# Optimization experiments

Hardware: AMD Instinct MI355X
Metric: run time of the kernel (lower is better)

## Reference

```python
import jax, jax.numpy as jnp
import numpy as np

C = 256
INTER = C // 2


def _conv1x1(x, w, b):
    # x: [B,C,H,W], w: [O,C], b: [O] -> [B,O,H,W]
    return jnp.einsum('bchw,oc->bohw', x, w) + b[None, :, None, None]


def setup_inputs() -> dict:
    key = jax.random.key(0)
    ks = jax.random.split(key, 9)
    B, H, W = 4, 64, 64
    x = jax.random.normal(ks[0], (B, C, H, W), dtype=jnp.float32)
    s_in = 1.0 / np.sqrt(C)
    s_int = 1.0 / np.sqrt(INTER)
    return {
        'x': x,
        'w_g': jax.random.normal(ks[1], (INTER, C), jnp.float32) * s_in,
        'b_g': jax.random.normal(ks[2], (INTER,), jnp.float32) * 0.01,
        'w_theta': jax.random.normal(ks[3], (INTER, C), jnp.float32) * s_in,
        'b_theta': jax.random.normal(ks[4], (INTER,), jnp.float32) * 0.01,
        'w_phi': jax.random.normal(ks[5], (INTER, C), jnp.float32) * s_in,
        'b_phi': jax.random.normal(ks[6], (INTER,), jnp.float32) * 0.01,
        'w_W': jax.random.normal(ks[7], (C, INTER), jnp.float32) * s_int,
        'b_W': jax.random.normal(ks[8], (C,), jnp.float32) * 0.01,
    }


def reference(x, w_g, b_g, w_theta, b_theta, w_phi, b_phi, w_W, b_W):
    B, Cc, H, W = x.shape
    N = H * W
    # 1x1 conv projections -> flatten spatial to N
    g_x = _conv1x1(x, w_g, b_g).reshape(B, INTER, N).transpose(0, 2, 1)        # [B,N,I]
    theta_x = _conv1x1(x, w_theta, b_theta).reshape(B, INTER, N).transpose(0, 2, 1)  # [B,N,I]
    phi_x = _conv1x1(x, w_phi, b_phi).reshape(B, INTER, N)                     # [B,I,N]
    f = jnp.einsum('bni,bim->bnm', theta_x, phi_x)                             # [B,N,N]
    f_div_C = jax.nn.softmax(f, axis=-1)
    y = jnp.einsum('bnm,bmi->bni', f_div_C, g_x)                               # [B,N,I]
    y = y.transpose(0, 2, 1).reshape(B, INTER, H, W)
    W_y = _conv1x1(y, w_W, b_W)                                                # [B,C,H,W]
    return W_y + x
```

## Files before the change

### kernel.cpp

```cpp
#include <hip/hip_runtime.h>

typedef unsigned short ushort_t;
typedef unsigned int uint_t;
typedef _Float16 f16;
typedef __attribute__((ext_vector_type(8))) _Float16 f16x8;
typedef __attribute__((ext_vector_type(2))) _Float16 f16x2;
typedef __attribute__((ext_vector_type(4))) float f32x4;

#define B_ 4
#define C_ 256
#define I_ 128
#define N_ 4096
#define SPLITS 4
#define KV_PER (N_ / SPLITS)
#define KVB 64
#define NIT (KV_PER / KVB)

#define XT_HI 0ull
#define XT_LO 4194304ull
#define W_F   8388608ull
#define TH_F  8519680ull
#define PH_F  10616832ull
#define G2_F  12713984ull
#define YP_OFF 0ull
#define YM_OFF TH_F
#define LSE_BYTE_OFF 29622272ull

__device__ __forceinline__ f16x2 pkrtz(float a, float b) {
    auto r = __builtin_amdgcn_cvt_pkrtz(a, b);
    f16x2 o;
    __builtin_memcpy(&o, &r, sizeof(o));
    return o;
}
__device__ __forceinline__ f32x4 mfma16h(f16x8 a, f16x8 b, f32x4 c) {
    return __builtin_amdgcn_mfma_f32_16x16x32_f16(a, b, c, 0, 0, 0);
}
__device__ __forceinline__ f32x4 zero4() { f32x4 z = {0.f, 0.f, 0.f, 0.f}; return z; }
__device__ __forceinline__ void gload_lds16(const void* g, void* lds) {
    __builtin_amdgcn_global_load_lds(
        (const __attribute__((address_space(1))) void*)g,
        (__attribute__((address_space(3))) void*)lds, 16, 0, 0);
}

__global__ __launch_bounds__(256) void k_convert_w(const float* wg, const float* wt,
                                                   const float* wp, const float* wW,
                                                   ushort_t* ws) {
    int idx = blockIdx.x * 256 + threadIdx.x;
    float v;
    if (idx < 32768)        v = wg[idx];
    else if (idx < 65536)   v = wt[idx - 32768];
    else if (idx < 98304)   v = wp[idx - 65536];
    else                    v = wW[idx - 98304];
    ((f16*)(ws + W_F))[idx] = (f16)v;
}

__global__ __launch_bounds__(256) void k_transpose_x(const float* x, ushort_t* ws) {
    __shared__ float t[64][65];
    int b = blockIdx.z, c0 = blockIdx.y * 64, n0 = blockIdx.x * 64;
    int tid = threadIdx.x;
    int cl = tid & 63, ng = tid >> 6;
    const float* xp = x + ((size_t)(b * C_ + c0 + cl)) * N_ + n0 + ng * 16;
#pragma unroll
    for (int j = 0; j < 4; ++j) {
        float4 v = ((const float4*)xp)[j];
        t[cl][ng * 16 + j * 4 + 0] = v.x;
        t[cl][ng * 16 + j * 4 + 1] = v.y;
        t[cl][ng * 16 + j * 4 + 2] = v.z;
        t[cl][ng * 16 + j * 4 + 3] = v.w;
    }
    __syncthreads();
    int nl = tid & 63, cg = tid >> 6;
    f16 hv[16], lv[16];
#pragma unroll
    for (int k = 0; k < 16; ++k) {
        float v = t[cg * 16 + k][nl];
        f16 h = (f16)v;
        hv[k] = h;
        lv[k] = (f16)(v - (float)h);
    }
    size_t dst = ((size_t)b * N_ + n0 + nl) * C_ + c0 + cg * 16;
    *(uint4*)&ws[XT_HI + dst]     = *(uint4*)&hv[0];
    *(uint4*)&ws[XT_HI + dst + 8] = *(uint4*)&hv[8];
    *(uint4*)&ws[XT_LO + dst]     = *(uint4*)&lv[0];
    *(uint4*)&ws[XT_LO + dst + 8] = *(uint4*)&lv[8];
}

__global__ __launch_bounds__(512) void k_proj_all(const float* bg, const float* bth,
                                                  const float* bph, ushort_t* ws) {
    int b = blockIdx.y, n0 = blockIdx.x * 64;
    int w = threadIdx.x >> 6, l = threadIdx.x & 63;
    int li = l & 15, lg = l >> 4;
    int wn = (w & 3) * 16;
    int ihb = (w >> 2) * 4;
    const f16* xh = (const f16*)(ws + XT_HI);
    const f16* xl = (const f16*)(ws + XT_LO);
    const f16* wf = (const f16*)(ws + W_F);

    f32x4 acc[3][4];
#pragma unroll
    for (int p = 0; p < 3; ++p)
#pragma unroll
        for (int t = 0; t < 4; ++t) acc[p][t] = zero4();

    size_t arow = ((size_t)b * N_ + n0 + wn + li) * C_;
#pragma unroll 2
    for (int kb = 0; kb < 8; ++kb) {
        int kc = kb * 32 + 8 * lg;
        f16x8 ah = *(const f16x8*)&xh[arow + kc];
        f16x8 al = *(const f16x8*)&xl[arow + kc];
#pragma unroll
        for (int p = 0; p < 3; ++p)
#pragma unroll
            for (int t = 0; t < 4; ++t) {
                f16x8 bw = *(const f16x8*)&wf[(size_t)p * 32768 + (size_t)((ihb + t) * 16 + li) * C_ + kc];
                acc[p][t] = mfma16h(ah, bw, acc[p][t]);
                acc[p][t] = mfma16h(al, bw, acc[p][t]);
            }
    }
    f16* g2p = (f16*)(ws + G2_F);
    f16* thp = (f16*)(ws + TH_F);
    f16* php = (f16*)(ws + PH_F);
#pragma unroll
    for (int p = 0; p < 3; ++p) {
        const float* bias = (p == 0) ? bg : (p == 1) ? bth : bph;
#pragma unroll
        for (int t = 0; t < 4; ++t) {
            int i = (ihb + t) * 16 + li;
            float bs = bias[i];
#pragma unroll
            for (int r = 0; r < 4; ++r) {
                int n = n0 + wn + 4 * lg + r;
                float v = acc[p][t][r] + bs;
                if (p == 0)
                    g2p[(((size_t)b * (N_ / 4) + (n >> 2)) * I_ + i) * 4 + (n & 3)] = (f16)v;
                else if (p == 1)
                    thp[((size_t)b * N_ + n) * I_ + i] = (f16)v;
                else
                    php[((size_t)b * N_ + n) * I_ + i] = (f16)v;
            }
        }
    }
}

__global__ __launch_bounds__(512, 4) void k_attn(ushort_t* ws, float* lse) {
    __shared__ __align__(16) ushort_t smem[32768];
    int b = blockIdx.y, sp = blockIdx.z;
    int w = threadIdx.x >> 6, l = threadIdx.x & 63;
    int li = l & 15, lg = l >> 4;
    int q0 = blockIdx.x * 128 + w * 16;
    const f16* th = (const f16*)(ws + TH_F);
    const f16* ph = (const f16*)(ws + PH_F);
    const f16* g2 = (const f16*)(ws + G2_F);
    f16* yp = (f16*)(ws + YP_OFF) + (size_t)sp * ((size_t)B_ * N_ * I_);

    f16x8 qf[4];
#pragma unroll
    for (int kb = 0; kb < 4; ++kb)
        qf[kb] = *(const f16x8*)&th[((size_t)b * N_ + q0 + li) * I_ + kb * 32 + 8 * lg];

    f32x4 y[8];
#pragma unroll
    for (int dt = 0; dt < 8; ++dt) y[dt] = zero4();
    float m = -1e30f, ls = 0.f;

    int kv_beg = sp * KV_PER;
    int srow = l >> 4;
    size_t sp0 = ((size_t)b * N_ + w * 8 + srow) * I_ + ((l & 15) ^ srow) * 8;
    size_t sp1 = ((size_t)b * N_ + w * 8 + 4 + srow) * I_ + (((l & 15) ^ srow) ^ 4) * 8;
    size_t sg0 = ((size_t)b * (N_ / 4) + w * 2) * (I_ * 4) + l * 8;
    int dp = w * 1024;
    int dg = 16384 + w * 1024;

    auto stage = [&](int kv0, int bufsel) {
        int bo = bufsel ? 8192 : 0;
        gload_lds16(ph + sp0 + (size_t)kv0 * I_, smem + bo + dp);
        gload_lds16(ph + sp1 + (size_t)kv0 * I_, smem + bo + dp + 512);
        gload_lds16(g2 + sg0 + (size_t)kv0 * 128, smem + bo + dg);
        gload_lds16(g2 + sg0 + (size_t)kv0 * 128 + 512, smem + bo + dg + 512);
    };

    stage(kv_beg, 0);
    __syncthreads();

    for (int it = 0; it < NIT; ++it) {
        int buf = it & 1;
        if (it + 1 < NIT) stage(kv_beg + (it + 1) * KVB, buf ^ 1);
        const f16* pbuf = (const f16*)(smem + (buf ? 8192 : 0));
        const f16* gbuf = (const f16*)(smem + 16384 + (buf ? 8192 : 0));

        f32x4 f[4];
#pragma unroll
        for (int h = 0; h < 4; ++h) f[h] = zero4();
        __builtin_amdgcn_s_setprio(1);
#pragma unroll
        for (int kb = 0; kb < 4; ++kb) {
            int cc = ((kb * 4 + lg) ^ (li & 7)) * 8;
#pragma unroll
            for (int h = 0; h < 4; ++h) {
                f16x8 a = *(const f16x8*)&pbuf[(h * 16 + li) * 128 + cc];
                f[h] = mfma16h(a, qf[kb], f[h]);
            }
        }
        __builtin_amdgcn_s_setprio(0);

        float tm = fmaxf(fmaxf(fmaxf(f[0][0], f[0][1]), fmaxf(f[0][2], f[0][3])),
                         fmaxf(fmaxf(f[1][0], f[1][1]), fmaxf(f[1][2], f[1][3])));
        tm = fmaxf(tm, fmaxf(fmaxf(fmaxf(f[2][0], f[2][1]), fmaxf(f[2][2], f[2][3])),
                             fmaxf(fmaxf(f[3][0], f[3][1]), fmaxf(f[3][2], f[3][3]))));
        tm = fmaxf(tm, __shfl_xor(tm, 16));
        tm = fmaxf(tm, __shfl_xor(tm, 32));
        if (__ballot(tm > m + 8.f)) {
            float mn = fmaxf(m, tm);
            float sc = __expf(m - mn);
            ls *= sc; m = mn;
            float s0 = __shfl(sc, 4 * lg + 0);
            float s1 = __shfl(sc, 4 * lg + 1);
            float s2 = __shfl(sc, 4 * lg + 2);
            float s3 = __shfl(sc, 4 * lg + 3);
#pragma unroll
            for (int dt = 0; dt < 8; ++dt) {
                y[dt][0] *= s0; y[dt][1] *= s1; y[dt][2] *= s2; y[dt][3] *= s3;
            }
        }
        float rs = 0.f;
#pragma unroll
        for (int h = 0; h < 4; ++h)
#pragma unroll
            for (int r = 0; r < 4; ++r) {
                f[h][r] = __expf(f[h][r] - m);
                rs += f[h][r];
            }
        rs += __shfl_xor(rs, 16);
        rs += __shfl_xor(rs, 32);
        ls += rs;

        union PU { f16x2 h2[4]; f16x8 v; };
        PU pA, pB;
        pA.h2[0] = pkrtz(f[0][0], f[0][1]); pA.h2[1] = pkrtz(f[0][2], f[0][3]);
        pA.h2[2] = pkrtz(f[1][0], f[1][1]); pA.h2[3] = pkrtz(f[1][2], f[1][3]);
        pB.h2[0] = pkrtz(f[2][0], f[2][1]); pB.h2[1] = pkrtz(f[2][2], f[2][3]);
        pB.h2[2] = pkrtz(f[3][0], f[3][1]); pB.h2[3] = pkrtz(f[3][2], f[3][3]);

        __builtin_amdgcn_s_setprio(1);
#pragma unroll
        for (int dt = 0; dt < 8; ++dt) {
            int i4 = (dt * 16 + li) * 4;
            union GU { uint_t u[4]; f16x8 v; };
            GU g0, g1;
            *(uint2*)&g0.u[0] = *(const uint2*)&gbuf[lg * 512 + i4];
            *(uint2*)&g0.u[2] = *(const uint2*)&gbuf[(4 + lg) * 512 + i4];
            y[dt] = mfma16h(pA.v, g0.v, y[dt]);
            *(uint2*)&g1.u[0] = *(const uint2*)&gbuf[(8 + lg) * 512 + i4];
            *(uint2*)&g1.u[2] = *(const uint2*)&gbuf[(12 + lg) * 512 + i4];
            y[dt] = mfma16h(pB.v, g1.v, y[dt]);
        }
        __builtin_amdgcn_s_setprio(0);
        __syncthreads();
    }

    float inv = 1.0f / ls;
    float i0 = __shfl(inv, 4 * lg + 0);
    float i1 = __shfl(inv, 4 * lg + 1);
    float i2 = __shfl(inv, 4 * lg + 2);
    float i3 = __shfl(inv, 4 * lg + 3);
#pragma unroll
    for (int dt = 0; dt < 8; ++dt) {
        size_t base = ((size_t)b * N_ + q0 + 4 * lg) * I_ + dt * 16 + li;
        yp[base]          = (f16)(y[dt][0] * i0);
        yp[base + I_]     = (f16)(y[dt][1] * i1);
        yp[base + 2 * I_] = (f16)(y[dt][2] * i2);
        yp[base + 3 * I_] = (f16)(y[dt][3] * i3);
    }
    if (l < 16)
        lse[((size_t)sp * B_ + b) * N_ + q0 + l] = m + __logf(ls);
}

__global__ __launch_bounds__(256) void k_merge(ushort_t* ws, const float* lse) {
    int t = blockIdx.x * 256 + threadIdx.x;
    size_t base = (size_t)t * 8;
    size_t row = base >> 7;
    float l0 = lse[row];
    float l1 = lse[(size_t)B_ * N_ + row];
    float l2 = lse[2 * (size_t)B_ * N_ + row];
    float l3 = lse[3 * (size_t)B_ * N_ + row];
    float mx = fmaxf(fmaxf(l0, l1), fmaxf(l2, l3));
    float w0 = __expf(l0 - mx), w1 = __expf(l1 - mx);
    float w2 = __expf(l2 - mx), w3 = __expf(l3 - mx);
    float inv = 1.0f / (w0 + w1 + w2 + w3);
    float wgt[4] = {w0 * inv, w1 * inv, w2 * inv, w3 * inv};
    const f16* yp = (const f16*)(ws + YP_OFF);
    const size_t STRIDE = (size_t)B_ * N_ * I_;
    float acc[8];
#pragma unroll
    for (int j = 0; j < 8; ++j) acc[j] = 0.f;
#pragma unroll
    for (int sp = 0; sp < 4; ++sp) {
        f16x8 v = *(const f16x8*)&yp[sp * STRIDE + base];
#pragma unroll
        for (int j = 0; j < 8; ++j) acc[j] += wgt[sp] * (float)v[j];
    }
    f16 o[8];
#pragma unroll
    for (int j = 0; j < 8; ++j) o[j] = (f16)acc[j];
    *(uint4*)&((f16*)(ws + YM_OFF))[base] = *(uint4*)&o[0];
}

__global__ __launch_bounds__(256) void k_out(const float* x, const float* bW,
                                             const ushort_t* ws, float* out) {
    int b = blockIdx.y, n0 = blockIdx.x * 64;
    int w = threadIdx.x >> 6, l = threadIdx.x & 63;
    int li = l & 15, lg = l >> 4;
    int cw = blockIdx.z * 128 + (w >> 1) * 64;
    int nh = (w & 1) * 32;
    const f16* wfp = (const f16*)(ws + W_F) + 98304;
    const f16* yb  = (const f16*)(ws + YM_OFF);

    f32x4 acc[4][2];
#pragma unroll
    for (int mm = 0; mm < 4; ++mm)
#pragma unroll
        for (int n = 0; n < 2; ++n) acc[mm][n] = zero4();

#pragma unroll 2
    for (int kb = 0; kb < 4; ++kb) {
        int kc = kb * 32 + 8 * lg;
        f16x8 a[4], byv[2];
#pragma unroll
        for (int mm = 0; mm < 4; ++mm)
            a[mm] = *(const f16x8*)&wfp[(size_t)(cw + mm * 16 + li) * I_ + kc];
#pragma unroll
        for (int n = 0; n < 2; ++n)
            byv[n] = *(const f16x8*)&yb[((size_t)b * N_ + n0 + nh + n * 16 + li) * I_ + kc];
#pragma unroll
        for (int mm = 0; mm < 4; ++mm)
#pragma unroll
            for (int n = 0; n < 2; ++n)
                acc[mm][n] = mfma16h(a[mm], byv[n], acc[mm][n]);
    }
#pragma unroll
    for (int mm = 0; mm < 4; ++mm)
#pragma unroll
        for (int n = 0; n < 2; ++n)
#pragma unroll
            for (int r = 0; r < 4; ++r) {
                int c = cw + mm * 16 + lg * 4 + r;
                int nn = n0 + nh + n * 16 + li;
                size_t xi = ((size_t)b * C_ + c) * N_ + nn;
                out[xi] = acc[mm][n][r] + bW[c] + x[xi];
            }
}

extern "C" void kernel_launch(void* const* d_in, const int* in_sizes, int n_in,
                              void* d_out, int out_size, void* d_ws, size_t ws_size,
                              hipStream_t stream) {
    const float* x  = (const float*)d_in[0];
    const float* wg = (const float*)d_in[1];
    const float* bg = (const float*)d_in[2];
    const float* wt = (const float*)d_in[3];
    const float* bt = (const float*)d_in[4];
    const float* wp = (const float*)d_in[5];
    const float* bp = (const float*)d_in[6];
    const float* wW = (const float*)d_in[7];
    const float* bW = (const float*)d_in[8];
    ushort_t* ws = (ushort_t*)d_ws;
    float* lse = (float*)((char*)d_ws + LSE_BYTE_OFF);
    float* out = (float*)d_out;

    k_convert_w<<<512, 256, 0, stream>>>(wg, wt, wp, wW, ws);
    k_transpose_x<<<dim3(64, 4, 4), 256, 0, stream>>>(x, ws);
    k_proj_all<<<dim3(64, 4), 512, 0, stream>>>(bg, bt, bp, ws);
    k_attn<<<dim3(32, 4, SPLITS), 512, 0, stream>>>(ws, lse);
    k_merge<<<1024, 256, 0, stream>>>(ws, lse);
    k_out<<<dim3(64, 4, 2), 256, 0, stream>>>(x, bW, ws, out);
}
```

Baseline: 119.6 us.

## Drop hi/lo x split, fuse weight convert and merge, retile attention with exp2

```diff
diff --git a/kernel.cpp b/kernel.cpp
--- a/kernel.cpp
+++ b/kernel.cpp
@@ -11,20 +11,18 @@
 #define C_ 256
 #define I_ 128
 #define N_ 4096
-#define SPLITS 4
-#define KV_PER (N_ / SPLITS)
-#define KVB 64
-#define NIT (KV_PER / KVB)
-
-#define XT_HI 0ull
-#define XT_LO 4194304ull
-#define W_F   8388608ull
-#define TH_F  8519680ull
-#define PH_F  10616832ull
-#define G2_F  12713984ull
-#define YP_OFF 0ull
-#define YM_OFF TH_F
-#define LSE_BYTE_OFF 29622272ull
+#define KVB 32
+#define LOG2E 1.44269504f
+
+#define XT_F 0ull
+#define W_F  4194304ull
+#define TH_F 4325376ull
+#define PH_F 6422528ull
+#define G2_F 8519680ull
+#define YP_F 10616832ull
+
+__device__ __forceinline__ float exp2_hw(float x) { return __builtin_amdgcn_exp2f(x); }
+__device__ __forceinline__ float log2_hw(float x) { return __builtin_amdgcn_logf(x); }
 
 __device__ __forceinline__ f16x2 pkrtz(float a, float b) {
     auto r = __builtin_amdgcn_cvt_pkrtz(a, b);
@@ -42,19 +40,25 @@
         (__attribute__((address_space(3))) void*)lds, 16, 0, 0);
 }
 
-__global__ __launch_bounds__(256) void k_convert_w(const float* wg, const float* wt,
-                                                   const float* wp, const float* wW,
-                                                   ushort_t* ws) {
-    int idx = blockIdx.x * 256 + threadIdx.x;
-    float v;
-    if (idx < 32768)        v = wg[idx];
-    else if (idx < 65536)   v = wt[idx - 32768];
-    else if (idx < 98304)   v = wp[idx - 65536];
-    else                    v = wW[idx - 98304];
-    ((f16*)(ws + W_F))[idx] = (f16)v;
-}
-
-__global__ __launch_bounds__(256) void k_transpose_x(const float* x, ushort_t* ws) {
+__global__ __launch_bounds__(256) void k_transpose_x(const float* x, const float* wg,
+        const float* wt, const float* wp, const float* wW, ushort_t* ws) {
+    if (blockIdx.x >= 64) {
+        int idx = (((blockIdx.x - 64) * 16 + blockIdx.y * 4 + blockIdx.z) * 256
+                   + threadIdx.x) * 16;
+        const float* src;
+        int off;
+        if (idx < 32768)      { src = wg; off = idx; }
+        else if (idx < 65536) { src = wt; off = idx - 32768; }
+        else if (idx < 98304) { src = wp; off = idx - 65536; }
+        else                  { src = wW; off = idx - 98304; }
+        f16 o[16];
+#pragma unroll
+        for (int j = 0; j < 16; ++j) o[j] = (f16)src[off + j];
+        f16* wd = (f16*)(ws + W_F);
+        *(uint4*)&wd[idx]     = *(uint4*)&o[0];
+        *(uint4*)&wd[idx + 8] = *(uint4*)&o[8];
+        return;
+    }
     __shared__ float t[64][65];
     int b = blockIdx.z, c0 = blockIdx.y * 64, n0 = blockIdx.x * 64;
     int tid = threadIdx.x;
@@ -70,19 +74,13 @@
     }
     __syncthreads();
     int nl = tid & 63, cg = tid >> 6;
-    f16 hv[16], lv[16];
-#pragma unroll
-    for (int k = 0; k < 16; ++k) {
-        float v = t[cg * 16 + k][nl];
-        f16 h = (f16)v;
-        hv[k] = h;
-        lv[k] = (f16)(v - (float)h);
-    }
+    f16 hv[16];
+#pragma unroll
+    for (int k = 0; k < 16; ++k) hv[k] = (f16)t[cg * 16 + k][nl];
     size_t dst = ((size_t)b * N_ + n0 + nl) * C_ + c0 + cg * 16;
-    *(uint4*)&ws[XT_HI + dst]     = *(uint4*)&hv[0];
-    *(uint4*)&ws[XT_HI + dst + 8] = *(uint4*)&hv[8];
-    *(uint4*)&ws[XT_LO + dst]     = *(uint4*)&lv[0];
-    *(uint4*)&ws[XT_LO + dst + 8] = *(uint4*)&lv[8];
+    f16* xd = (f16*)(ws + XT_F);
+    *(uint4*)&xd[dst]     = *(uint4*)&hv[0];
+    *(uint4*)&xd[dst + 8] = *(uint4*)&hv[8];
 }
 
 __global__ __launch_bounds__(512) void k_proj_all(const float* bg, const float* bth,
@@ -92,8 +90,7 @@
     int li = l & 15, lg = l >> 4;
     int wn = (w & 3) * 16;
     int ihb = (w >> 2) * 4;
-    const f16* xh = (const f16*)(ws + XT_HI);
-    const f16* xl = (const f16*)(ws + XT_LO);
+    const f16* xh = (const f16*)(ws + XT_F);
     const f16* wf = (const f16*)(ws + W_F);
 
     f32x4 acc[3][4];
@@ -107,14 +104,13 @@
     for (int kb = 0; kb < 8; ++kb) {
         int kc = kb * 32 + 8 * lg;
         f16x8 ah = *(const f16x8*)&xh[arow + kc];
-        f16x8 al = *(const f16x8*)&xl[arow + kc];
 #pragma unroll
         for (int p = 0; p < 3; ++p)
 #pragma unroll
             for (int t = 0; t < 4; ++t) {
-                f16x8 bw = *(const f16x8*)&wf[(size_t)p * 32768 + (size_t)((ihb + t) * 16 + li) * C_ + kc];
+                f16x8 bw = *(const f16x8*)&wf[(size_t)p * 32768
+                               + (size_t)((ihb + t) * 16 + li) * C_ + kc];
                 acc[p][t] = mfma16h(ah, bw, acc[p][t]);
-                acc[p][t] = mfma16h(al, bw, acc[p][t]);
             }
     }
     f16* g2p = (f16*)(ws + G2_F);
@@ -134,7 +130,7 @@
                 if (p == 0)
                     g2p[(((size_t)b * (N_ / 4) + (n >> 2)) * I_ + i) * 4 + (n & 3)] = (f16)v;
                 else if (p == 1)
-                    thp[((size_t)b * N_ + n) * I_ + i] = (f16)v;
+                    thp[((size_t)b * N_ + n) * I_ + i] = (f16)(v * LOG2E);
                 else
                     php[((size_t)b * N_ + n) * I_ + i] = (f16)v;
             }
@@ -142,8 +138,8 @@
     }
 }
 
-__global__ __launch_bounds__(512, 4) void k_attn(ushort_t* ws, float* lse) {
-    __shared__ __align__(16) ushort_t smem[32768];
+__global__ __launch_bounds__(256, 3) void k_attn(ushort_t* ws, float* lse, int splits) {
+    __shared__ __align__(16) ushort_t smem[16384];
     int b = blockIdx.y, sp = blockIdx.z;
     int w = threadIdx.x >> 6, l = threadIdx.x & 63;
     int li = l & 15, lg = l >> 4;
@@ -151,175 +147,219 @@
     const f16* th = (const f16*)(ws + TH_F);
     const f16* ph = (const f16*)(ws + PH_F);
     const f16* g2 = (const f16*)(ws + G2_F);
-    f16* yp = (f16*)(ws + YP_OFF) + (size_t)sp * ((size_t)B_ * N_ * I_);
-
-    f16x8 qf[4];
-#pragma unroll
-    for (int kb = 0; kb < 4; ++kb)
-        qf[kb] = *(const f16x8*)&th[((size_t)b * N_ + q0 + li) * I_ + kb * 32 + 8 * lg];
-
-    f32x4 y[8];
-#pragma unroll
-    for (int dt = 0; dt < 8; ++dt) y[dt] = zero4();
-    float m = -1e30f, ls = 0.f;
-
-    int kv_beg = sp * KV_PER;
+    f16* yp = (f16*)(ws + YP_F) + (size_t)sp * ((size_t)B_ * N_ * I_);
+
+    f16x8 qA[4], qB[4];
+#pragma unroll
+    for (int kb = 0; kb < 4; ++kb) {
+        qA[kb] = *(const f16x8*)&th[((size_t)b * N_ + q0 + li) * I_ + kb * 32 + 8 * lg];
+        qB[kb] = *(const f16x8*)&th[((size_t)b * N_ + q0 + 64 + li) * I_ + kb * 32 + 8 * lg];
+    }
+
+    f32x4 yA[8], yB[8];
+#pragma unroll
+    for (int dt = 0; dt < 8; ++dt) { yA[dt] = zero4(); yB[dt] = zero4(); }
+    float mA = -1e30f, lA = 0.f, mB = -1e30f, lB = 0.f;
+
+    int kvper = N_ / splits;
+    int kv_beg = sp * kvper, nit = kvper / KVB;
     int srow = l >> 4;
     size_t sp0 = ((size_t)b * N_ + w * 8 + srow) * I_ + ((l & 15) ^ srow) * 8;
     size_t sp1 = ((size_t)b * N_ + w * 8 + 4 + srow) * I_ + (((l & 15) ^ srow) ^ 4) * 8;
-    size_t sg0 = ((size_t)b * (N_ / 4) + w * 2) * (I_ * 4) + l * 8;
-    int dp = w * 1024;
-    int dg = 16384 + w * 1024;
+    size_t sg0 = ((size_t)b * (N_ / 4) + w * 2) * 512 + l * 8;
 
     auto stage = [&](int kv0, int bufsel) {
-        int bo = bufsel ? 8192 : 0;
-        gload_lds16(ph + sp0 + (size_t)kv0 * I_, smem + bo + dp);
-        gload_lds16(ph + sp1 + (size_t)kv0 * I_, smem + bo + dp + 512);
-        gload_lds16(g2 + sg0 + (size_t)kv0 * 128, smem + bo + dg);
-        gload_lds16(g2 + sg0 + (size_t)kv0 * 128 + 512, smem + bo + dg + 512);
+        int bo = bufsel * 4096;
+        gload_lds16(ph + (size_t)kv0 * I_ + sp0, smem + bo + w * 1024);
+        gload_lds16(ph + (size_t)kv0 * I_ + sp1, smem + bo + w * 1024 + 512);
+        gload_lds16(g2 + (size_t)(kv0 >> 2) * 512 + sg0, smem + 8192 + bo + w * 1024);
+        gload_lds16(g2 + (size_t)(kv0 >> 2) * 512 + sg0 + 512,
+                    smem + 8192 + bo + w * 1024 + 512);
     };
 
     stage(kv_beg, 0);
     __syncthreads();
 
-    for (int it = 0; it < NIT; ++it) {
+    for (int it = 0; it < nit; ++it) {
         int buf = it & 1;
-        if (it + 1 < NIT) stage(kv_beg + (it + 1) * KVB, buf ^ 1);
-        const f16* pbuf = (const f16*)(smem + (buf ? 8192 : 0));
-        const f16* gbuf = (const f16*)(smem + 16384 + (buf ? 8192 : 0));
-
-        f32x4 f[4];
-#pragma unroll
-        for (int h = 0; h < 4; ++h) f[h] = zero4();
+        if (it + 1 < nit) stage(kv_beg + (it + 1) * KVB, buf ^ 1);
+        const f16* pb = (const f16*)(smem + buf * 4096);
+        const f16* gbf = (const f16*)(smem + 8192 + buf * 4096);
+
+        f32x4 fA0 = zero4(), fA1 = zero4(), fB0 = zero4(), fB1 = zero4();
         __builtin_amdgcn_s_setprio(1);
 #pragma unroll
         for (int kb = 0; kb < 4; ++kb) {
             int cc = ((kb * 4 + lg) ^ (li & 7)) * 8;
-#pragma unroll
-            for (int h = 0; h < 4; ++h) {
-                f16x8 a = *(const f16x8*)&pbuf[(h * 16 + li) * 128 + cc];
-                f[h] = mfma16h(a, qf[kb], f[h]);
-            }
+            f16x8 a0 = *(const f16x8*)&pb[li * 128 + cc];
+            f16x8 a1 = *(const f16x8*)&pb[(16 + li) * 128 + cc];
+            fA0 = mfma16h(a0, qA[kb], fA0);
+            fB0 = mfma16h(a0, qB[kb], fB0);
+            fA1 = mfma16h(a1, qA[kb], fA1);
+            fB1 = mfma16h(a1, qB[kb], fB1);
         }
         __builtin_amdgcn_s_setprio(0);
 
-        float tm = fmaxf(fmaxf(fmaxf(f[0][0], f[0][1]), fmaxf(f[0][2], f[0][3])),
-                         fmaxf(fmaxf(f[1][0], f[1][1]), fmaxf(f[1][2], f[1][3])));
-        tm = fmaxf(tm, fmaxf(fmaxf(fmaxf(f[2][0], f[2][1]), fmaxf(f[2][2], f[2][3])),
-                             fmaxf(fmaxf(f[3][0], f[3][1]), fmaxf(f[3][2], f[3][3]))));
-        tm = fmaxf(tm, __shfl_xor(tm, 16));
-        tm = fmaxf(tm, __shfl_xor(tm, 32));
-        if (__ballot(tm > m + 8.f)) {
-            float mn = fmaxf(m, tm);
-            float sc = __expf(m - mn);
-            ls *= sc; m = mn;
+        float tmA = fmaxf(fmaxf(fmaxf(fA0[0], fA0[1]), fmaxf(fA0[2], fA0[3])),
+                          fmaxf(fmaxf(fA1[0], fA1[1]), fmaxf(fA1[2], fA1[3])));
+        tmA = fmaxf(tmA, __shfl_xor(tmA, 16));
+        tmA = fmaxf(tmA, __shfl_xor(tmA, 32));
+        if (__ballot(tmA > mA + 11.0f)) {
+            float mn = fmaxf(mA, tmA);
+            float sc = exp2_hw(mA - mn);
+            lA *= sc; mA = mn;
             float s0 = __shfl(sc, 4 * lg + 0);
             float s1 = __shfl(sc, 4 * lg + 1);
             float s2 = __shfl(sc, 4 * lg + 2);
             float s3 = __shfl(sc, 4 * lg + 3);
 #pragma unroll
             for (int dt = 0; dt < 8; ++dt) {
-                y[dt][0] *= s0; y[dt][1] *= s1; y[dt][2] *= s2; y[dt][3] *= s3;
-            }
-        }
-        float rs = 0.f;
-#pragma unroll
-        for (int h = 0; h < 4; ++h)
-#pragma unroll
-            for (int r = 0; r < 4; ++r) {
-                f[h][r] = __expf(f[h][r] - m);
-                rs += f[h][r];
-            }
-        rs += __shfl_xor(rs, 16);
-        rs += __shfl_xor(rs, 32);
-        ls += rs;
-
+                yA[dt][0] *= s0; yA[dt][1] *= s1; yA[dt][2] *= s2; yA[dt][3] *= s3;
+            }
+        }
+        float rsA = 0.f;
+#pragma unroll
+        for (int r = 0; r < 4; ++r) {
+            fA0[r] = exp2_hw(fA0[r] - mA); rsA += fA0[r];
+            fA1[r] = exp2_hw(fA1[r] - mA); rsA += fA1[r];
+        }
+        rsA += __shfl_xor(rsA, 16);
+        rsA += __shfl_xor(rsA, 32);
+        lA += rsA;
         union PU { f16x2 h2[4]; f16x8 v; };
-        PU pA, pB;
-        pA.h2[0] = pkrtz(f[0][0], f[0][1]); pA.h2[1] = pkrtz(f[0][2], f[0][3]);
-        pA.h2[2] = pkrtz(f[1][0], f[1][1]); pA.h2[3] = pkrtz(f[1][2], f[1][3]);
-        pB.h2[0] = pkrtz(f[2][0], f[2][1]); pB.h2[1] = pkrtz(f[2][2], f[2][3]);
-        pB.h2[2] = pkrtz(f[3][0], f[3][1]); pB.h2[3] = pkrtz(f[3][2], f[3][3]);
+        PU pA;
+        pA.h2[0] = pkrtz(fA0[0], fA0[1]); pA.h2[1] = pkrtz(fA0[2], fA0[3]);
+        pA.h2[2] = pkrtz(fA1[0], fA1[1]); pA.h2[3] = pkrtz(fA1[2], fA1[3]);
+
+        float tmB = fmaxf(fmaxf(fmaxf(fB0[0], fB0[1]), fmaxf(fB0[2], fB0[3])),
+                          fmaxf(fmaxf(fB1[0], fB1[1]), fmaxf(fB1[2], fB1[3])));
+        tmB = fmaxf(tmB, __shfl_xor(tmB, 16));
+        tmB = fmaxf(tmB, __shfl_xor(tmB, 32));
+        if (__ballot(tmB > mB + 11.0f)) {
+            float mn = fmaxf(mB, tmB);
+            float sc = exp2_hw(mB - mn);
+            lB *= sc; mB = mn;
+            float s0 = __shfl(sc, 4 * lg + 0);
+            float s1 = __shfl(sc, 4 * lg + 1);
+            float s2 = __shfl(sc, 4 * lg + 2);
+            float s3 = __shfl(sc, 4 * lg + 3);
+#pragma unroll
+            for (int dt = 0; dt < 8; ++dt) {
+                yB[dt][0] *= s0; yB[dt][1] *= s1; yB[dt][2] *= s2; yB[dt][3] *= s3;
+            }
+        }
+        float rsB = 0.f;
+#pragma unroll
+        for (int r = 0; r < 4; ++r) {
+            fB0[r] = exp2_hw(fB0[r] - mB); rsB += fB0[r];
+            fB1[r] = exp2_hw(fB1[r] - mB); rsB += fB1[r];
+        }
+        rsB += __shfl_xor(rsB, 16);
+        rsB += __shfl_xor(rsB, 32);
+        lB += rsB;
+        PU pB;
+        pB.h2[0] = pkrtz(fB0[0], fB0[1]); pB.h2[1] = pkrtz(fB0[2], fB0[3]);
+        pB.h2[2] = pkrtz(fB1[0], fB1[1]); pB.h2[3] = pkrtz(fB1[2], fB1[3]);
 
         __builtin_amdgcn_s_setprio(1);
 #pragma unroll
         for (int dt = 0; dt < 8; ++dt) {
-            int i4 = (dt * 16 + li) * 4;
-            union GU { uint_t u[4]; f16x8 v; };
-            GU g0, g1;
-            *(uint2*)&g0.u[0] = *(const uint2*)&gbuf[lg * 512 + i4];
-            *(uint2*)&g0.u[2] = *(const uint2*)&gbuf[(4 + lg) * 512 + i4];
-            y[dt] = mfma16h(pA.v, g0.v, y[dt]);
-            *(uint2*)&g1.u[0] = *(const uint2*)&gbuf[(8 + lg) * 512 + i4];
-            *(uint2*)&g1.u[2] = *(const uint2*)&gbuf[(12 + lg) * 512 + i4];
-            y[dt] = mfma16h(pB.v, g1.v, y[dt]);
+            int gi = (dt * 16 + li) * 4;
+            uint2 ga = *(const uint2*)&gbf[lg * 512 + gi];
+            uint2 gbv = *(const uint2*)&gbf[(4 + lg) * 512 + gi];
+            union { uint_t u[4]; f16x8 v; } gu;
+            gu.u[0] = ga.x; gu.u[1] = ga.y; gu.u[2] = gbv.x; gu.u[3] = gbv.y;
+            yA[dt] = mfma16h(pA.v, gu.v, yA[dt]);
+            yB[dt] = mfma16h(pB.v, gu.v, yB[dt]);
         }
         __builtin_amdgcn_s_setprio(0);
         __syncthreads();
     }
 
-    float inv = 1.0f / ls;
-    float i0 = __shfl(inv, 4 * lg + 0);
-    float i1 = __shfl(inv, 4 * lg + 1);
-    float i2 = __shfl(inv, 4 * lg + 2);
-    float i3 = __shfl(inv, 4 * lg + 3);
-#pragma unroll
-    for (int dt = 0; dt < 8; ++dt) {
-        size_t base = ((size_t)b * N_ + q0 + 4 * lg) * I_ + dt * 16 + li;
-        yp[base]          = (f16)(y[dt][0] * i0);
-        yp[base + I_]     = (f16)(y[dt][1] * i1);
-        yp[base + 2 * I_] = (f16)(y[dt][2] * i2);
-        yp[base + 3 * I_] = (f16)(y[dt][3] * i3);
-    }
-    if (l < 16)
-        lse[((size_t)sp * B_ + b) * N_ + q0 + l] = m + __logf(ls);
-}
-
-__global__ __launch_bounds__(256) void k_merge(ushort_t* ws, const float* lse) {
-    int t = blockIdx.x * 256 + threadIdx.x;
-    size_t base = (size_t)t * 8;
-    size_t row = base >> 7;
-    float l0 = lse[row];
-    float l1 = lse[(size_t)B_ * N_ + row];
-    float l2 = lse[2 * (size_t)B_ * N_ + row];
-    float l3 = lse[3 * (size_t)B_ * N_ + row];
-    float mx = fmaxf(fmaxf(l0, l1), fmaxf(l2, l3));
-    float w0 = __expf(l0 - mx), w1 = __expf(l1 - mx);
-    float w2 = __expf(l2 - mx), w3 = __expf(l3 - mx);
-    float inv = 1.0f / (w0 + w1 + w2 + w3);
-    float wgt[4] = {w0 * inv, w1 * inv, w2 * inv, w3 * inv};
-    const f16* yp = (const f16*)(ws + YP_OFF);
-    const size_t STRIDE = (size_t)B_ * N_ * I_;
-    float acc[8];
-#pragma unroll
-    for (int j = 0; j < 8; ++j) acc[j] = 0.f;
-#pragma unroll
-    for (int sp = 0; sp < 4; ++sp) {
-        f16x8 v = *(const f16x8*)&yp[sp * STRIDE + base];
-#pragma unroll
-        for (int j = 0; j < 8; ++j) acc[j] += wgt[sp] * (float)v[j];
-    }
-    f16 o[8];
-#pragma unroll
-    for (int j = 0; j < 8; ++j) o[j] = (f16)acc[j];
-    *(uint4*)&((f16*)(ws + YM_OFF))[base] = *(uint4*)&o[0];
-}
-
-__global__ __launch_bounds__(256) void k_out(const float* x, const float* bW,
-                                             const ushort_t* ws, float* out) {
+    {
+        float inv = 1.0f / lA;
+        float i0 = __shfl(inv, 4 * lg + 0);
+        float i1 = __shfl(inv, 4 * lg + 1);
+        float i2 = __shfl(inv, 4 * lg + 2);
+        float i3 = __shfl(inv, 4 * lg + 3);
+#pragma unroll
+        for (int dt = 0; dt < 8; ++dt) {
+            size_t base = ((size_t)b * N_ + q0 + 4 * lg) * I_ + dt * 16 + li;
+            yp[base]          = (f16)(yA[dt][0] * i0);
+            yp[base + I_]     = (f16)(yA[dt][1] * i1);
+            yp[base + 2 * I_] = (f16)(yA[dt][2] * i2);
+            yp[base + 3 * I_] = (f16)(yA[dt][3] * i3);
+        }
+    }
+    {
+        float inv = 1.0f / lB;
+        float i0 = __shfl(inv, 4 * lg + 0);
+        float i1 = __shfl(inv, 4 * lg + 1);
+        float i2 = __shfl(inv, 4 * lg + 2);
+        float i3 = __shfl(inv, 4 * lg + 3);
+#pragma unroll
+        for (int dt = 0; dt < 8; ++dt) {
+            size_t base = ((size_t)b * N_ + q0 + 64 + 4 * lg) * I_ + dt * 16 + li;
+            yp[base]          = (f16)(yB[dt][0] * i0);
+            yp[base + I_]     = (f16)(yB[dt][1] * i1);
+            yp[base + 2 * I_] = (f16)(yB[dt][2] * i2);
+            yp[base + 3 * I_] = (f16)(yB[dt][3] * i3);
+        }
+    }
+    if (l < 16) {
+        lse[((size_t)sp * B_ + b) * N_ + q0 + l]      = mA + log2_hw(lA);
+        lse[((size_t)sp * B_ + b) * N_ + q0 + 64 + l] = mB + log2_hw(lB);
+    }
+}
+
+__global__ __launch_bounds__(512) void k_out(const float* x, const float* bW,
+        const ushort_t* ws, const float* lse, float* out, int splits) {
+    __shared__ __align__(16) f16 ylds[64 * 136];
     int b = blockIdx.y, n0 = blockIdx.x * 64;
-    int w = threadIdx.x >> 6, l = threadIdx.x & 63;
+    int tid = threadIdx.x;
+    {
+        int nn = tid >> 3, ig = tid & 7;
+        size_t lrow = (size_t)b * N_ + n0 + nn;
+        float mx = -1e30f;
+        for (int s = 0; s < splits; ++s)
+            mx = fmaxf(mx, lse[(size_t)s * (B_ * N_) + lrow]);
+        float sum = 0.f;
+        for (int s = 0; s < splits; ++s)
+            sum += exp2_hw(lse[(size_t)s * (B_ * N_) + lrow] - mx);
+        float inv = 1.0f / sum;
+        float acc[16];
+#pragma unroll
+        for (int j = 0; j < 16; ++j) acc[j] = 0.f;
+        const f16* ypb = (const f16*)(ws + YP_F);
+        for (int s = 0; s < splits; ++s) {
+            float wg = exp2_hw(lse[(size_t)s * (B_ * N_) + lrow] - mx) * inv;
+            const f16* p = ypb + (size_t)s * ((size_t)B_ * N_ * I_) + lrow * I_ + ig * 16;
+            f16x8 v0 = *(const f16x8*)p;
+            f16x8 v1 = *(const f16x8*)(p + 8);
+#pragma unroll
+            for (int j = 0; j < 8; ++j) {
+                acc[j]     += wg * (float)v0[j];
+                acc[8 + j] += wg * (float)v1[j];
+            }
+        }
+        f16 o[16];
+#pragma unroll
+        for (int j = 0; j < 16; ++j) o[j] = (f16)acc[j];
+        *(uint4*)&ylds[nn * 136 + ig * 16]     = *(uint4*)&o[0];
+        *(uint4*)&ylds[nn * 136 + ig * 16 + 8] = *(uint4*)&o[8];
+    }
+    __syncthreads();
+
+    int w = tid >> 6, l = tid & 63;
     int li = l & 15, lg = l >> 4;
-    int cw = blockIdx.z * 128 + (w >> 1) * 64;
-    int nh = (w & 1) * 32;
+    int cw = (w >> 1) * 64, nh = (w & 1) * 32;
     const f16* wfp = (const f16*)(ws + W_F) + 98304;
-    const f16* yb  = (const f16*)(ws + YM_OFF);
-
-    f32x4 acc[4][2];
+
+    f32x4 acc2[4][2];
 #pragma unroll
     for (int mm = 0; mm < 4; ++mm)
 #pragma unroll
-        for (int n = 0; n < 2; ++n) acc[mm][n] = zero4();
+        for (int n = 0; n < 2; ++n) acc2[mm][n] = zero4();
 
 #pragma unroll 2
     for (int kb = 0; kb < 4; ++kb) {
@@ -330,12 +370,12 @@
             a[mm] = *(const f16x8*)&wfp[(size_t)(cw + mm * 16 + li) * I_ + kc];
 #pragma unroll
         for (int n = 0; n < 2; ++n)
-            byv[n] = *(const f16x8*)&yb[((size_t)b * N_ + n0 + nh + n * 16 + li) * I_ + kc];
+            byv[n] = *(const f16x8*)&ylds[(nh + n * 16 + li) * 136 + kc];
 #pragma unroll
         for (int mm = 0; mm < 4; ++mm)
 #pragma unroll
             for (int n = 0; n < 2; ++n)
-                acc[mm][n] = mfma16h(a[mm], byv[n], acc[mm][n]);
+                acc2[mm][n] = mfma16h(a[mm], byv[n], acc2[mm][n]);
     }
 #pragma unroll
     for (int mm = 0; mm < 4; ++mm)
@@ -346,7 +386,7 @@
                 int c = cw + mm * 16 + lg * 4 + r;
                 int nn = n0 + nh + n * 16 + li;
                 size_t xi = ((size_t)b * C_ + c) * N_ + nn;
-                out[xi] = acc[mm][n][r] + bW[c] + x[xi];
+                out[xi] = acc2[mm][n][r] + bW[c] + x[xi];
             }
 }
 
@@ -363,13 +403,14 @@
     const float* wW = (const float*)d_in[7];
     const float* bW = (const float*)d_in[8];
     ushort_t* ws = (ushort_t*)d_ws;
-    float* lse = (float*)((char*)d_ws + LSE_BYTE_OFF);
     float* out = (float*)d_out;
 
-    k_convert_w<<<512, 256, 0, stream>>>(wg, wt, wp, wW, ws);
-    k_transpose_x<<<dim3(64, 4, 4), 256, 0, stream>>>(x, ws);
+    int splits = (ws_size >= 55400000ull) ? 8 : 4;
+    size_t lse_off = 2ull * (YP_F + (size_t)splits * 2097152ull);
+    float* lse = (float*)((char*)d_ws + lse_off);
+
+    k_transpose_x<<<dim3(66, 4, 4), 256, 0, stream>>>(x, wg, wt, wp, wW, ws);
     k_proj_all<<<dim3(64, 4), 512, 0, stream>>>(bg, bt, bp, ws);
-    k_attn<<<dim3(32, 4, SPLITS), 512, 0, stream>>>(ws, lse);
-    k_merge<<<1024, 256, 0, stream>>>(ws, lse);
-    k_out<<<dim3(64, 4, 2), 256, 0, stream>>>(x, bW, ws, out);
-}
+    k_attn<<<dim3(32, 4, splits), 256, 0, stream>>>(ws, lse, splits);
+    k_out<<<dim3(64, 4), 512, 0, stream>>>(x, bW, ws, lse, out, splits);
+}
```

Result: no change. 117.9 us (-1.5%).
